# Kernel optimization log

Hardware: AMD Instinct MI355X
Metric: run time of the kernel (lower is better)

The kernel has to match this reference:

```python
import jax, jax.numpy as jnp
import numpy as np

B, T, I, O = 128, 512, 700, 128  # batch, nb_steps, input_size, output_size
TIME_STEP, TAU_SYN, TAU_MEM, GAMMA_SHAPE = 1e-3, 10e-3, 20e-3, 3.0


def setup_inputs() -> dict:
    key = jax.random.key(0)
    k1, k2 = jax.random.split(key)
    inputs = jax.random.normal(k1, (B, T, I), dtype=jnp.float32)
    bound = 1.0 / np.sqrt(I)  # kaiming-uniform-like fan_in bound
    w = jax.random.uniform(k2, (I, O), minval=-bound, maxval=bound, dtype=jnp.float32)
    # heterogeneous per-neuron decay constants (het_ab=True), frozen params
    rng = np.random.default_rng(0)
    alpha = jnp.asarray(np.exp(-TIME_STEP / rng.gamma(GAMMA_SHAPE, TAU_SYN / GAMMA_SHAPE, (1, O))), dtype=jnp.float32)
    beta = jnp.asarray(np.exp(-TIME_STEP / rng.gamma(GAMMA_SHAPE, TAU_MEM / GAMMA_SHAPE, (1, O))), dtype=jnp.float32)
    return {"inputs": inputs, "w": w, "alpha": alpha, "beta": beta}


def reference(inputs, w, alpha, beta):
    # h: (B, T, O)
    h = jnp.einsum('btc,cd->btd', inputs, w)
    Bh, Th, Oh = h.shape
    zeros = jnp.zeros((Bh, Oh), dtype=h.dtype)
    one_minus_beta = 1.0 - beta  # beta is frozen, detach is a no-op here

    def step(carry, ht):
        syn, mem = carry
        new_syn = alpha * syn + ht
        new_mem = beta * mem + one_minus_beta * syn  # uses OLD syn
        return (new_syn, new_mem), (new_syn, new_mem)

    # scan over the first T-1 timesteps (time-major)
    h_tm = jnp.swapaxes(h[:, :Th - 1], 0, 1)  # (T-1, B, O)
    _, (syn_seq, mem_seq) = jax.lax.scan(step, (zeros, zeros), h_tm)
    syn_rec = jnp.concatenate([zeros[:, None], jnp.swapaxes(syn_seq, 0, 1)], axis=1)  # (B, T, O)
    mem_rec = jnp.concatenate([zeros[:, None], jnp.swapaxes(mem_seq, 0, 1)], axis=1)
    return (syn_rec, mem_rec)
```

## Files before the change

kernel.cpp:

```cpp
#include <hip/hip_runtime.h>
#include <hip/hip_bf16.h>
#include <stdint.h>

#define Bsz 128
#define Tn  512
#define In  700
#define On  128
#define Mn  (Bsz * Tn)
#define KP  704
#define NSEG 16
#define LSEG 32
#define BO   (Bsz * On)
#define NKT  22

using bf16x8 = __attribute__((ext_vector_type(8))) short;
using f32x4  = __attribute__((ext_vector_type(4))) float;

#define WAITVM(N) asm volatile("s_waitcnt vmcnt(" #N ")" ::: "memory")

__device__ __forceinline__ uint32_t f2bf(float f) {
  union { float f; uint32_t u; } v; v.f = f;
  return (v.u + 0x7fffu + ((v.u >> 16) & 1u)) >> 16;
}

__device__ __forceinline__ bf16x8 cvt8(float4 f0, float4 f1) {
  bf16x8 r;
  r[0] = (short)f2bf(f0.x); r[1] = (short)f2bf(f0.y);
  r[2] = (short)f2bf(f0.z); r[3] = (short)f2bf(f0.w);
  r[4] = (short)f2bf(f1.x); r[5] = (short)f2bf(f1.y);
  r[6] = (short)f2bf(f1.z); r[7] = (short)f2bf(f1.w);
  return r;
}

__device__ __forceinline__ void gload16(const void* g, void* l) {
  __builtin_amdgcn_global_load_lds(
      (__attribute__((address_space(1))) void*)g,
      (__attribute__((address_space(3))) void*)l, 16, 0, 0);
}

__global__ void prep_wt(const float* __restrict__ w, ushort* __restrict__ w_t) {
  int idx = blockIdx.x * 256 + threadIdx.x;
  if (idx >= On * KP) return;
  int col = idx / KP, k = idx - col * KP;
  float v = (k < In) ? w[(size_t)k * On + col] : 0.0f;
  w_t[(size_t)col * KP + k] = (ushort)f2bf(v);
}

union SMU {
  struct {
    uint32_t A[3][4096];
    uint32_t B[3][2048];
  } db;
  float sc[128 * 132];
};

__global__ __launch_bounds__(256, 2) void gemm_h(
    const float* __restrict__ A,
    const ushort* __restrict__ Wt,
    float* __restrict__ H,
    float2* __restrict__ ep,
    const float* __restrict__ alpha, const float* __restrict__ beta)
{
  __shared__ __align__(16) SMU sm;

  const int tid  = threadIdx.x;
  const int bm   = blockIdx.x;
  const int lane = tid & 63;
  const int wid  = tid >> 6;
  const int wm   = wid >> 1, wn = wid & 1;
  const int l16  = lane & 15, lkb = lane >> 4;

  const int   o_ep = tid & 127;
  const float a_ep = alpha[o_ep];
  const float b_ep = beta[o_ep];

  f32x4 acc[4][4];
#pragma unroll
  for (int i = 0; i < 4; ++i)
#pragma unroll
    for (int n = 0; n < 4; ++n) acc[i][n] = (f32x4){0.f, 0.f, 0.f, 0.f};

  auto stage = [&](int bi, int kt) {
    const int k0 = kt * 32;
#pragma unroll
    for (int is = 0; is < 4; ++is) {
      const int q   = is * 256 + wid * 64 + lane;
      const int row = q >> 3, sl = q & 7;
      int gk = k0 + ((sl ^ (row & 7)) << 2);
      if (gk >= In) gk = k0;
      gload16(A + (size_t)(bm * 128 + row) * In + gk,
              &sm.db.A[bi][is * 1024 + wid * 256]);
    }
#pragma unroll
    for (int is = 0; is < 2; ++is) {
      const int q   = is * 256 + wid * 64 + lane;
      const int col = q >> 2, sl = q & 3;
      const int ks  = sl ^ ((col >> 1) & 3);
      gload16(Wt + (size_t)col * KP + k0 + ks * 8,
              &sm.db.B[bi][is * 1024 + wid * 256]);
    }
  };

  auto tile = [&](int kt, int cur) {
    __builtin_amdgcn_s_barrier();
    const float4* Af = (const float4*)sm.db.A[cur];
    const bf16x8* Bf = (const bf16x8*)sm.db.B[cur];
    bf16x8 af[4], bfr[4];
#pragma unroll
    for (int i = 0; i < 4; ++i) {
      const int row = wm * 64 + i * 16 + l16;
      const int s0  = (lkb * 2) ^ (row & 7);
      const int s1  = (lkb * 2 + 1) ^ (row & 7);
      af[i] = cvt8(Af[row * 8 + s0], Af[row * 8 + s1]);
    }
#pragma unroll
    for (int n = 0; n < 4; ++n) {
      const int col = wn * 64 + n * 16 + l16;
      bfr[n] = Bf[col * 4 + (lkb ^ ((col >> 1) & 3))];
    }
    asm volatile("s_waitcnt lgkmcnt(0)" ::: "memory");
    __builtin_amdgcn_s_barrier();
    if (kt + 3 < NKT) stage(cur, kt + 3);
#pragma unroll
    for (int i = 0; i < 4; ++i)
#pragma unroll
      for (int n = 0; n < 4; ++n)
        acc[i][n] = __builtin_amdgcn_mfma_f32_16x16x32_bf16(af[i], bfr[n], acc[i][n], 0, 0, 0);
  };

  stage(0, 0); stage(1, 1); stage(2, 2);
  {
    int cur = 0;
    for (int kt = 0; kt < NKT - 2; ++kt) {
      WAITVM(12);
      tile(kt, cur);
      cur = (cur == 2) ? 0 : cur + 1;
    }
    WAITVM(6);  tile(NKT - 2, (NKT - 2) % 3);
    WAITVM(0);  tile(NKT - 1, (NKT - 1) % 3);
  }

#pragma unroll
  for (int i = 0; i < 4; ++i)
#pragma unroll
    for (int n = 0; n < 4; ++n) {
      const int col = wn * 64 + n * 16 + l16;
#pragma unroll
      for (int r = 0; r < 4; ++r) {
        const int row = wm * 64 + i * 16 + lkb * 4 + r;
        sm.sc[row * 132 + col] = acc[i][n][r];
      }
    }
  __syncthreads();

  const size_t hbase = (size_t)bm * 128 * 128;
#pragma unroll
  for (int i2 = 0; i2 < 16; ++i2) {
    const int q = i2 * 256 + tid;
    const int row = q >> 5, v = q & 31;
    *(float4*)&H[hbase + row * 128 + v * 4] =
        *(const float4*)&sm.sc[row * 132 + v * 4];
  }

  if (ep) {
    const float a = a_ep, bt = b_ep, omb = 1.0f - b_ep;
    const int b = bm >> 2, seg0 = (bm & 3) * 4;
#pragma unroll
    for (int cc = 0; cc < 2; ++cc) {
      const int sl = (tid >> 7) + cc * 2;
      float S = 0.f, M = 0.f;
      const float* base = &sm.sc[(sl * 32) * 132 + o_ep];
#pragma unroll
      for (int t = 0; t < 32; ++t) {
        const float x = base[t * 132];
        M = fmaf(bt, M, omb * S);
        S = fmaf(a, S, x);
      }
      ep[(size_t)(seg0 + sl) * BO + b * On + o_ep] = make_float2(S, M);
    }
  }
}

__global__ __launch_bounds__(256) void scan_seg(
    float* __restrict__ syn, float* __restrict__ mem, const float2* __restrict__ ep,
    const float* __restrict__ alpha, const float* __restrict__ beta)
{
  const int cid = blockIdx.x * 256 + threadIdx.x;
  const int o   = cid & (On - 1);
  const int bs  = cid >> 7;
  const int seg = bs & (NSEG - 1), b = bs >> 4;
  const float a = alpha[o], bt = beta[o], omb = 1.0f - bt;

  float aL = 1.f, bL = 1.f, cL = 0.f;
#pragma unroll
  for (int i = 0; i < LSEG; ++i) {
    cL = fmaf(bt, cL, omb * aL);
    aL *= a; bL *= bt;
  }
  float S = 0.f, M = 0.f;
  for (int j = 0; j < seg; ++j) {
    const float2 e = ep[(size_t)j * BO + b * On + o];
    const float nS = fmaf(aL, S, e.x);
    M = fmaf(bL, M, fmaf(cL, S, e.y));
    S = nS;
  }

  float* hp = syn + ((size_t)b * Tn + seg * LSEG) * On + o;
  float* mp = mem + ((size_t)b * Tn + seg * LSEG) * On + o;
  float buf[8];
#pragma unroll
  for (int d = 0; d < 8; ++d) buf[d] = hp[d * On];
  for (int tb = 0; tb < LSEG; tb += 8) {
#pragma unroll
    for (int d = 0; d < 8; ++d) {
      const int t = tb + d;
      const float x = buf[d];
      if (t + 8 < LSEG) buf[d] = hp[(t + 8) * On];
      hp[t * On] = S;
      mp[t * On] = M;
      M = fmaf(bt, M, omb * S);
      S = fmaf(a, S, x);
    }
  }
}

__global__ __launch_bounds__(64) void scan_k(
    float* __restrict__ syn, float* __restrict__ mem,
    const float* __restrict__ alpha, const float* __restrict__ beta)
{
  const int b = blockIdx.x >> 1;
  const int o = ((blockIdx.x & 1) << 6) + threadIdx.x;
  const float a = alpha[o], bt = beta[o], omb = 1.0f - bt;
  float* hp = syn + (size_t)b * Tn * On + o;
  float* mp = mem + (size_t)b * Tn * On + o;
  float S = 0.f, M = 0.f;
  float buf[8];
#pragma unroll
  for (int d = 0; d < 8; ++d) buf[d] = hp[d * On];
  for (int tb = 0; tb < Tn; tb += 8) {
#pragma unroll
    for (int d = 0; d < 8; ++d) {
      const int t = tb + d;
      const float h_t = buf[d];
      if (t + 8 < Tn) buf[d] = hp[(t + 8) * On];
      hp[t * On] = S;
      mp[t * On] = M;
      const float nS = fmaf(a, S, h_t);
      M = fmaf(bt, M, omb * S);
      S = nS;
    }
  }
}

extern "C" void kernel_launch(void* const* d_in, const int* in_sizes, int n_in,
                              void* d_out, int out_size, void* d_ws, size_t ws_size,
                              hipStream_t stream) {
  const float* inputs = (const float*)d_in[0];
  const float* w      = (const float*)d_in[1];
  const float* alpha  = (const float*)d_in[2];
  const float* beta   = (const float*)d_in[3];

  float* syn = (float*)d_out;
  float* mem = syn + (size_t)Bsz * Tn * On;
  ushort* w_t = (ushort*)mem;

  const size_t ep_bytes = (size_t)NSEG * BO * sizeof(float2);
  float2* ep = (ws_size >= ep_bytes) ? (float2*)d_ws : nullptr;

  prep_wt<<<(On * KP + 255) / 256, 256, 0, stream>>>(w, w_t);
  gemm_h<<<Mn / 128, 256, 0, stream>>>(inputs, w_t, syn, ep, alpha, beta);

  if (ep) {
    scan_seg<<<(Bsz * NSEG * On) / 256, 256, 0, stream>>>(syn, mem, ep, alpha, beta);
  } else {
    scan_k<<<Bsz * 2, 64, 0, stream>>>(syn, mem, alpha, beta);
  }
}
```

Baseline: 63.07 us.

## Fuse GEMM and segmented scan into one cooperative kernel with grid sync

```diff
diff --git a/kernel.cpp b/kernel.cpp
--- a/kernel.cpp
+++ b/kernel.cpp
@@ -1,6 +1,9 @@
 #include <hip/hip_runtime.h>
 #include <hip/hip_bf16.h>
+#include <hip/hip_cooperative_groups.h>
 #include <stdint.h>
+
+namespace cg = cooperative_groups;
 
 #define Bsz 128
 #define Tn  512
@@ -24,12 +27,12 @@
 }
 
 __device__ __forceinline__ bf16x8 cvt8(float4 f0, float4 f1) {
-  bf16x8 r;
-  r[0] = (short)f2bf(f0.x); r[1] = (short)f2bf(f0.y);
-  r[2] = (short)f2bf(f0.z); r[3] = (short)f2bf(f0.w);
-  r[4] = (short)f2bf(f1.x); r[5] = (short)f2bf(f1.y);
-  r[6] = (short)f2bf(f1.z); r[7] = (short)f2bf(f1.w);
-  return r;
+  union { __hip_bfloat162 h2[4]; bf16x8 v; } u;
+  u.h2[0] = __float22bfloat162_rn(make_float2(f0.x, f0.y));
+  u.h2[1] = __float22bfloat162_rn(make_float2(f0.z, f0.w));
+  u.h2[2] = __float22bfloat162_rn(make_float2(f1.x, f1.y));
+  u.h2[3] = __float22bfloat162_rn(make_float2(f1.z, f1.w));
+  return u.v;
 }
 
 __device__ __forceinline__ void gload16(const void* g, void* l) {
@@ -54,10 +57,10 @@
   float sc[128 * 132];
 };
 
-__global__ __launch_bounds__(256, 2) void gemm_h(
+__global__ __launch_bounds__(256, 2) void fused_k(
     const float* __restrict__ A,
     const ushort* __restrict__ Wt,
-    float* __restrict__ H,
+    float* __restrict__ syn, float* __restrict__ mem,
     float2* __restrict__ ep,
     const float* __restrict__ alpha, const float* __restrict__ beta)
 {
@@ -73,6 +76,168 @@
   const int   o_ep = tid & 127;
   const float a_ep = alpha[o_ep];
   const float b_ep = beta[o_ep];
+  WAITVM(0);
+  __builtin_amdgcn_sched_barrier(0);
+
+  f32x4 acc[4][4];
+#pragma unroll
+  for (int i = 0; i < 4; ++i)
+#pragma unroll
+    for (int n = 0; n < 4; ++n) acc[i][n] = (f32x4){0.f, 0.f, 0.f, 0.f};
+
+  auto stage = [&](int bi, int kt) {
+    const int k0 = kt * 32;
+#pragma unroll
+    for (int is = 0; is < 4; ++is) {
+      const int q   = is * 256 + wid * 64 + lane;
+      const int row = q >> 3, sl = q & 7;
+      int gk = k0 + ((sl ^ (row & 7)) << 2);
+      if (gk >= In) gk = k0;
+      gload16(A + (size_t)(bm * 128 + row) * In + gk,
+              &sm.db.A[bi][is * 1024 + wid * 256]);
+    }
+#pragma unroll
+    for (int is = 0; is < 2; ++is) {
+      const int q   = is * 256 + wid * 64 + lane;
+      const int col = q >> 2, sl = q & 3;
+      const int ks  = sl ^ ((col >> 1) & 3);
+      gload16(Wt + (size_t)col * KP + k0 + ks * 8,
+              &sm.db.B[bi][is * 1024 + wid * 256]);
+    }
+  };
+
+  auto tile = [&](int kt, int cur) {
+    __builtin_amdgcn_s_barrier();
+    const float4* Af = (const float4*)sm.db.A[cur];
+    const bf16x8* Bf = (const bf16x8*)sm.db.B[cur];
+    bf16x8 af[4], bfr[4];
+#pragma unroll
+    for (int i = 0; i < 4; ++i) {
+      const int row = wm * 64 + i * 16 + l16;
+      const int s0  = (lkb * 2) ^ (row & 7);
+      const int s1  = (lkb * 2 + 1) ^ (row & 7);
+      af[i] = cvt8(Af[row * 8 + s0], Af[row * 8 + s1]);
+    }
+#pragma unroll
+    for (int n = 0; n < 4; ++n) {
+      const int col = wn * 64 + n * 16 + l16;
+      bfr[n] = Bf[col * 4 + (lkb ^ ((col >> 1) & 3))];
+    }
+    asm volatile("s_waitcnt lgkmcnt(0)" ::: "memory");
+    __builtin_amdgcn_s_barrier();
+    if (kt + 3 < NKT) stage(cur, kt + 3);
+#pragma unroll
+    for (int i = 0; i < 4; ++i)
+#pragma unroll
+      for (int n = 0; n < 4; ++n)
+        acc[i][n] = __builtin_amdgcn_mfma_f32_16x16x32_bf16(af[i], bfr[n], acc[i][n], 0, 0, 0);
+  };
+
+  stage(0, 0); stage(1, 1); stage(2, 2);
+  {
+    int cur = 0;
+    for (int kt = 0; kt < NKT - 2; ++kt) {
+      WAITVM(12);
+      tile(kt, cur);
+      cur = (cur == 2) ? 0 : cur + 1;
+    }
+    WAITVM(6);  tile(NKT - 2, (NKT - 2) % 3);
+    WAITVM(0);  tile(NKT - 1, (NKT - 1) % 3);
+  }
+
+#pragma unroll
+  for (int i = 0; i < 4; ++i)
+#pragma unroll
+    for (int n = 0; n < 4; ++n) {
+      const int col = wn * 64 + n * 16 + l16;
+#pragma unroll
+      for (int r = 0; r < 4; ++r) {
+        const int row = wm * 64 + i * 16 + lkb * 4 + r;
+        sm.sc[row * 132 + col] = acc[i][n][r];
+      }
+    }
+  __syncthreads();
+
+  {
+    const float a = a_ep, bt = b_ep, omb = 1.0f - b_ep;
+    const int b = bm >> 2, seg0 = (bm & 3) * 4;
+#pragma unroll
+    for (int cc = 0; cc < 2; ++cc) {
+      const int sl = (tid >> 7) + cc * 2;
+      float S = 0.f, M = 0.f;
+      const float* base = &sm.sc[(sl * 32) * 132 + o_ep];
+#pragma unroll
+      for (int t = 0; t < 32; ++t) {
+        const float x = base[t * 132];
+        M = fmaf(bt, M, omb * S);
+        S = fmaf(a, S, x);
+      }
+      ep[(size_t)(seg0 + sl) * BO + b * On + o_ep] = make_float2(S, M);
+    }
+  }
+
+  const int w    = wid;
+  const int gseg = (bm & 3) * 4 + w;
+  const int bb   = bm >> 2;
+  const float2 al2 = *(const float2*)&alpha[2 * lane];
+  const float2 be2 = *(const float2*)&beta[2 * lane];
+  const float a0 = al2.x, a1 = al2.y, b0 = be2.x, b1 = be2.y;
+  const float ob0 = 1.f - b0, ob1 = 1.f - b1;
+  float aL0 = 1.f, bL0 = 1.f, cL0 = 0.f, aL1 = 1.f, bL1 = 1.f, cL1 = 0.f;
+#pragma unroll
+  for (int i = 0; i < LSEG; ++i) {
+    cL0 = fmaf(b0, cL0, ob0 * aL0); aL0 *= a0; bL0 *= b0;
+    cL1 = fmaf(b1, cL1, ob1 * aL1); aL1 *= a1; bL1 *= b1;
+  }
+
+  __threadfence();
+  cg::this_grid().sync();
+
+  float S0 = 0.f, M0 = 0.f, S1 = 0.f, M1 = 0.f;
+#pragma unroll
+  for (int j = 0; j < NSEG - 1; ++j) {
+    const float4 E = *(const float4*)&ep[(size_t)j * BO + bb * On + 2 * lane];
+    if (j < gseg) {
+      const float nS0 = fmaf(aL0, S0, E.x);
+      M0 = fmaf(bL0, M0, fmaf(cL0, S0, E.y));
+      S0 = nS0;
+      const float nS1 = fmaf(aL1, S1, E.z);
+      M1 = fmaf(bL1, M1, fmaf(cL1, S1, E.w));
+      S1 = nS1;
+    }
+  }
+
+  const float* scb = &sm.sc[(w * 32) * 132 + 2 * lane];
+  float* sp = syn + ((size_t)bb * Tn + gseg * LSEG) * On + 2 * lane;
+  float* mp = mem + ((size_t)bb * Tn + gseg * LSEG) * On + 2 * lane;
+#pragma unroll
+  for (int t = 0; t < LSEG; ++t) {
+    const float2 x = *(const float2*)&scb[t * 132];
+    *(float2*)&sp[(size_t)t * On] = make_float2(S0, S1);
+    *(float2*)&mp[(size_t)t * On] = make_float2(M0, M1);
+    M0 = fmaf(b0, M0, ob0 * S0); S0 = fmaf(a0, S0, x.x);
+    M1 = fmaf(b1, M1, ob1 * S1); S1 = fmaf(a1, S1, x.y);
+  }
+}
+
+__global__ __launch_bounds__(256, 2) void gemm_h(
+    const float* __restrict__ A, const ushort* __restrict__ Wt,
+    float* __restrict__ H, float2* __restrict__ ep,
+    const float* __restrict__ alpha, const float* __restrict__ beta)
+{
+  __shared__ __align__(16) SMU sm;
+  const int tid  = threadIdx.x;
+  const int bm   = blockIdx.x;
+  const int lane = tid & 63;
+  const int wid  = tid >> 6;
+  const int wm   = wid >> 1, wn = wid & 1;
+  const int l16  = lane & 15, lkb = lane >> 4;
+
+  const int   o_ep = tid & 127;
+  const float a_ep = alpha[o_ep];
+  const float b_ep = beta[o_ep];
+  WAITVM(0);
+  __builtin_amdgcn_sched_barrier(0);
 
   f32x4 acc[4][4];
 #pragma unroll
@@ -268,11 +433,21 @@
   float2* ep = (ws_size >= ep_bytes) ? (float2*)d_ws : nullptr;
 
   prep_wt<<<(On * KP + 255) / 256, 256, 0, stream>>>(w, w_t);
-  gemm_h<<<Mn / 128, 256, 0, stream>>>(inputs, w_t, syn, ep, alpha, beta);
-
+
+  bool done = false;
   if (ep) {
-    scan_seg<<<(Bsz * NSEG * On) / 256, 256, 0, stream>>>(syn, mem, ep, alpha, beta);
-  } else {
-    scan_k<<<Bsz * 2, 64, 0, stream>>>(syn, mem, alpha, beta);
-  }
-}
+    void* args[7] = { (void*)&inputs, (void*)&w_t, (void*)&syn, (void*)&mem,
+                      (void*)&ep, (void*)&alpha, (void*)&beta };
+    hipError_t e = hipLaunchCooperativeKernel((const void*)fused_k,
+                                              dim3(Mn / 128), dim3(256),
+                                              args, 0, stream);
+    if (e == hipSuccess) done = true;
+    else (void)hipGetLastError();
+  }
+
+  if (!done) {
+    gemm_h<<<Mn / 128, 256, 0, stream>>>(inputs, w_t, syn, ep, alpha, beta);
+    if (ep) scan_seg<<<(Bsz * NSEG * On) / 256, 256, 0, stream>>>(syn, mem, ep, alpha, beta);
+    else    scan_k<<<Bsz * 2, 64, 0, stream>>>(syn, mem, alpha, beta);
+  }
+}
```

Measured after the change: 167.8 us. 166% more time.
